# Kernel tuning notes

Measured on AMD Instinct MI355X. Metric: run time of the kernel, lower is better.

## Reference

```python
import jax, jax.numpy as jnp
import numpy as np

EPS = 1e-5  # torch LayerNorm default


def setup_inputs() -> dict:
    key = jax.random.key(0)
    ks = jax.random.split(key, 12)
    N, D, F = 4096, 1024, 4096
    s = 1.0 / np.sqrt(D)
    sf = 1.0 / np.sqrt(F)
    return {
        "embeddings": jax.random.normal(ks[0], (N, D), dtype=jnp.float32),
        "Wq": jax.random.normal(ks[1], (D, D), dtype=jnp.float32) * s,
        "bq": jnp.zeros((D,), jnp.float32),
        "Wk": jax.random.normal(ks[2], (D, D), dtype=jnp.float32) * s,
        "bk": jnp.zeros((D,), jnp.float32),
        "Wv": jax.random.normal(ks[3], (D, D), dtype=jnp.float32) * s,
        "bv": jnp.zeros((D,), jnp.float32),
        "gamma": jnp.ones((D,), jnp.float32),
        "beta": jnp.zeros((D,), jnp.float32),
        "W1": jax.random.normal(ks[4], (D, F), dtype=jnp.float32) * s,
        "b1": jnp.zeros((F,), jnp.float32),
        "W2": jax.random.normal(ks[5], (F, D), dtype=jnp.float32) * sf,
        "b2": jnp.zeros((D,), jnp.float32),
    }


def reference(embeddings, Wq, bq, Wk, bk, Wv, bv, gamma, beta, W1, b1, W2, b2):
    N, D = embeddings.shape
    scale = jnp.sqrt(jnp.float32(D))  # embed_dim ** 0.5
    Q = embeddings @ Wq + bq          # [N, D]
    K = embeddings @ Wk + bk
    V = embeddings @ Wv + bv
    attn = (Q @ K.T) / scale          # [N, N]
    # causal mask: strictly upper triangle -> -inf
    causal = jnp.tril(jnp.ones((N, N), dtype=bool))
    attn = jnp.where(causal, attn, -jnp.inf)
    A = jax.nn.softmax(attn, axis=-1)
    attn_emb = A @ V                  # [N, D]  (dropout = identity at eval)
    # add & norm (LayerNorm over last dim)
    x = attn_emb + embeddings
    mu = jnp.mean(x, axis=-1, keepdims=True)
    var = jnp.mean((x - mu) ** 2, axis=-1, keepdims=True)
    x = (x - mu) / jnp.sqrt(var + EPS) * gamma + beta
    # FFN (no residual after ff in the original module)
    h = jax.nn.relu(x @ W1 + b1)
    return h @ W2 + b2
```

## Files before the change

kernel.cpp:

```cpp
#include <hip/hip_runtime.h>
#include <stdint.h>


using short8 = __attribute__((ext_vector_type(8))) short;
using f32x4  = __attribute__((ext_vector_type(4))) float;

__device__ __forceinline__ uint16_t f2bf(float f) {
  uint32_t u = __builtin_bit_cast(uint32_t, f);
  u += 0x7FFFu + ((u >> 16) & 1u);
  return (uint16_t)(u >> 16);
}

__device__ __forceinline__ void gload_lds16(const uint16_t* g, uint16_t* l) {
  __builtin_amdgcn_global_load_lds(
      (__attribute__((address_space(1))) void*)(void*)g,
      (__attribute__((address_space(3))) void*)l, 16, 0, 0);
}


__global__ __launch_bounds__(256) void gemm_qkv(
    const uint16_t* __restrict__ A, const uint16_t* __restrict__ Bt,
    const float* __restrict__ bias, uint16_t* __restrict__ Cout,
    uint16_t* __restrict__ Vt)
{
  constexpr int BK = 64;
  __shared__ uint16_t As[128 * BK];
  __shared__ uint16_t Bs[128 * BK];
  int id = blockIdx.x;
  int bm = id & 31, bn = id >> 5;
  bool vblk = (bn >= 16);

  int tid  = threadIdx.x;
  int lane = tid & 63;
  int wave = tid >> 6;
  int wm = (wave >> 1) * 64, wn = (wave & 1) * 64;
  int lr = lane & 15, quad = lane >> 4;

  const uint16_t *Ag[4], *Bg[4];
  uint16_t *Al[4], *Bl[4];
#pragma unroll
  for (int s = 0; s < 4; ++s) {
    int c = tid + 256 * s;
    int r = c >> 3, q = (c & 7) ^ (r & 7);
    Ag[s] = A  + (size_t)(bm * 128 + r) * 1024 + q * 8;
    Bg[s] = Bt + (size_t)(bn * 128 + r) * 1024 + q * 8;
    Al[s] = As + c * 8;
    Bl[s] = Bs + c * 8;
  }
  const uint16_t* Fa = vblk ? Bs : As;
  const uint16_t* Fb = vblk ? As : Bs;

  f32x4 acc[4][4] = {};

  for (int k0 = 0; k0 < 1024; k0 += BK) {
    __syncthreads();
#pragma unroll
    for (int s = 0; s < 4; ++s) gload_lds16(Ag[s] + k0, Al[s]);
#pragma unroll
    for (int s = 0; s < 4; ++s) gload_lds16(Bg[s] + k0, Bl[s]);
    __syncthreads();
#pragma unroll
    for (int h = 0; h < 2; ++h) {
      short8 af[4], bfr[4];
      int cc = quad + 4 * h;
#pragma unroll
      for (int i = 0; i < 4; ++i) {
        int r = wm + i * 16 + lr;
        af[i] = *(const short8*)(&Fa[(r * 8 + (cc ^ (r & 7))) * 8]);
      }
#pragma unroll
      for (int j = 0; j < 4; ++j) {
        int r = wn + j * 16 + lr;
        bfr[j] = *(const short8*)(&Fb[(r * 8 + (cc ^ (r & 7))) * 8]);
      }
#pragma unroll
      for (int i = 0; i < 4; ++i)
#pragma unroll
        for (int j = 0; j < 4; ++j)
          acc[i][j] = __builtin_amdgcn_mfma_f32_16x16x32_bf16(af[i], bfr[j], acc[i][j], 0, 0, 0);
    }
  }

  if (vblk) {
#pragma unroll
    for (int i = 0; i < 4; ++i) {
#pragma unroll
      for (int r = 0; r < 4; ++r) {
        int n = bn * 128 + wm + i * 16 + quad * 4 + r;
        float bv = bias[n];
        uint16_t* dst = Vt + (size_t)(n - 2048) * 4096 + bm * 128;
#pragma unroll
        for (int j = 0; j < 4; ++j)
          dst[wn + j * 16 + lr] = f2bf(acc[i][j][r] + bv);
      }
    }
  } else {
    int row0 = bm * 128 + wm + quad * 4;
    int col0 = bn * 128 + wn + lr;
#pragma unroll
    for (int j = 0; j < 4; ++j) {
      int col = col0 + j * 16;
      float bv = bias[col];
#pragma unroll
      for (int i = 0; i < 4; ++i)
#pragma unroll
        for (int r = 0; r < 4; ++r)
          Cout[(size_t)(row0 + i * 16 + r) * 3072 + col] = f2bf(acc[i][j][r] + bv);
    }
  }
}

__global__ __launch_bounds__(256) void gemm_ffn1(
    const uint16_t* __restrict__ A, const uint16_t* __restrict__ Bt,
    const float* __restrict__ bias, uint16_t* __restrict__ Cout)
{
  constexpr int BK = 64;
  __shared__ uint16_t As[128 * BK];
  __shared__ uint16_t Bs[128 * BK];
  int id = blockIdx.x;
  int bm = id & 31, bn = id >> 5;

  int tid  = threadIdx.x;
  int lane = tid & 63;
  int wave = tid >> 6;
  int wm = (wave >> 1) * 64, wn = (wave & 1) * 64;
  int lr = lane & 15, quad = lane >> 4;

  const uint16_t *Ag[4], *Bg[4];
  uint16_t *Al[4], *Bl[4];
#pragma unroll
  for (int s = 0; s < 4; ++s) {
    int c = tid + 256 * s;
    int r = c >> 3, q = (c & 7) ^ (r & 7);
    Ag[s] = A  + (size_t)(bm * 128 + r) * 1024 + q * 8;
    Bg[s] = Bt + (size_t)(bn * 128 + r) * 1024 + q * 8;
    Al[s] = As + c * 8;
    Bl[s] = Bs + c * 8;
  }

  f32x4 acc[4][4] = {};

  for (int k0 = 0; k0 < 1024; k0 += BK) {
    __syncthreads();
#pragma unroll
    for (int s = 0; s < 4; ++s) gload_lds16(Ag[s] + k0, Al[s]);
#pragma unroll
    for (int s = 0; s < 4; ++s) gload_lds16(Bg[s] + k0, Bl[s]);
    __syncthreads();
#pragma unroll
    for (int h = 0; h < 2; ++h) {
      short8 af[4], bfr[4];
      int cc = quad + 4 * h;
#pragma unroll
      for (int i = 0; i < 4; ++i) {
        int r = wm + i * 16 + lr;
        af[i] = *(const short8*)(&As[(r * 8 + (cc ^ (r & 7))) * 8]);
      }
#pragma unroll
      for (int j = 0; j < 4; ++j) {
        int r = wn + j * 16 + lr;
        bfr[j] = *(const short8*)(&Bs[(r * 8 + (cc ^ (r & 7))) * 8]);
      }
#pragma unroll
      for (int i = 0; i < 4; ++i)
#pragma unroll
        for (int j = 0; j < 4; ++j)
          acc[i][j] = __builtin_amdgcn_mfma_f32_16x16x32_bf16(af[i], bfr[j], acc[i][j], 0, 0, 0);
    }
  }

  int row0 = bm * 128 + wm + quad * 4;
  int col0 = bn * 128 + wn + lr;
#pragma unroll
  for (int j = 0; j < 4; ++j) {
    int col = col0 + j * 16;
    float bv = bias[col];
#pragma unroll
    for (int i = 0; i < 4; ++i)
#pragma unroll
      for (int r = 0; r < 4; ++r)
        Cout[(size_t)(row0 + i * 16 + r) * 4096 + col] =
            f2bf(fmaxf(acc[i][j][r] + bv, 0.0f));
  }
}

__global__ __launch_bounds__(256) void gemm_s(
    const uint16_t* __restrict__ Qm, const uint16_t* __restrict__ Km,
    uint16_t* __restrict__ Sb, float* __restrict__ lvec,
    int lda, int ldb, int ldc, float scale)
{
  constexpr int BK = 64;
  __shared__ uint16_t As[64 * BK];
  __shared__ uint16_t Bs[128 * BK];
  int id = blockIdx.x;
  int i64 = id & 63, bn = id >> 6;
  if (bn > (i64 >> 1)) return;

  int tid  = threadIdx.x;
  int lane = tid & 63;
  int wave = tid >> 6;
  int wm = (wave >> 1) * 32, wn = (wave & 1) * 64;
  int lr = lane & 15, quad = lane >> 4;

  const uint16_t *Ag[2], *Bg[4];
  uint16_t *Al[2], *Bl[4];
#pragma unroll
  for (int s = 0; s < 2; ++s) {
    int c = tid + 256 * s;
    int r = c >> 3, q = (c & 7) ^ (r & 7);
    Ag[s] = Qm + (size_t)(i64 * 64 + r) * lda + q * 8;
    Al[s] = As + c * 8;
  }
#pragma unroll
  for (int s = 0; s < 4; ++s) {
    int c = tid + 256 * s;
    int r = c >> 3, q = (c & 7) ^ (r & 7);
    Bg[s] = Km + (size_t)(bn * 128 + r) * ldb + q * 8;
    Bl[s] = Bs + c * 8;
  }

  f32x4 acc[2][4] = {};

  for (int k0 = 0; k0 < 1024; k0 += BK) {
    __syncthreads();
#pragma unroll
    for (int s = 0; s < 2; ++s) gload_lds16(Ag[s] + k0, Al[s]);
#pragma unroll
    for (int s = 0; s < 4; ++s) gload_lds16(Bg[s] + k0, Bl[s]);
    __syncthreads();
#pragma unroll
    for (int h = 0; h < 2; ++h) {
      short8 af[2], bfr[4];
      int cc = quad + 4 * h;
#pragma unroll
      for (int i = 0; i < 2; ++i) {
        int r = wm + i * 16 + lr;
        af[i] = *(const short8*)(&As[(r * 8 + (cc ^ (r & 7))) * 8]);
      }
#pragma unroll
      for (int j = 0; j < 4; ++j) {
        int r = wn + j * 16 + lr;
        bfr[j] = *(const short8*)(&Bs[(r * 8 + (cc ^ (r & 7))) * 8]);
      }
#pragma unroll
      for (int i = 0; i < 2; ++i)
#pragma unroll
        for (int j = 0; j < 4; ++j)
          acc[i][j] = __builtin_amdgcn_mfma_f32_16x16x32_bf16(af[i], bfr[j], acc[i][j], 0, 0, 0);
    }
  }

  int row0 = i64 * 64 + wm + quad * 4;
  int col0 = bn * 128 + wn + lr;
#pragma unroll
  for (int i = 0; i < 2; ++i) {
#pragma unroll
    for (int r = 0; r < 4; ++r) {
      int row = row0 + i * 16 + r;
      float s = 0.0f;
#pragma unroll
      for (int j = 0; j < 4; ++j) {
        int col = col0 + j * 16;
        float v = (col <= row) ? __expf(acc[i][j][r] * scale) : 0.0f;
        Sb[(size_t)row * ldc + col] = f2bf(v);
        s += v;
      }
#pragma unroll
      for (int o = 8; o > 0; o >>= 1) s += __shfl_xor(s, o, 64);
      if (lr == 0) unsafeAtomicAdd(&lvec[row], s);
    }
  }
}

__global__ __launch_bounds__(256) void gemm_o(
    const uint16_t* __restrict__ Sb, const uint16_t* __restrict__ Vt,
    float* __restrict__ Opart)
{
  constexpr int BK = 64;
  __shared__ uint16_t As[128 * BK];
  __shared__ uint16_t Bs[128 * BK];
  int id = blockIdx.x;
  int bn = id / 80, p = id % 80;
  int c, bm;
  if      (p < 25) { c = 0; bm = 7 + p; }
  else if (p < 49) { c = 1; bm = 8 + (p - 25); }
  else if (p < 65) { c = 2; bm = 16 + (p - 49); }
  else if (p < 73) { c = 3; bm = 24 + (p - 65); }
  else             { c = 0; bm = 79 - p; }
  int klo = c << 10;
  int khi = (bm + 1) << 7; if (khi > ((c + 1) << 10)) khi = (c + 1) << 10;

  int tid  = threadIdx.x;
  int lane = tid & 63;
  int wave = tid >> 6;
  int wm = (wave >> 1) * 64, wn = (wave & 1) * 64;
  int lr = lane & 15, quad = lane >> 4;

  const uint16_t *Ag[4], *Bg[4];
  uint16_t *Al[4], *Bl[4];
#pragma unroll
  for (int s = 0; s < 4; ++s) {
    int cch = tid + 256 * s;
    int r = cch >> 3, q = (cch & 7) ^ (r & 7);
    Ag[s] = Sb + (size_t)(bm * 128 + r) * 4096 + q * 8;
    Bg[s] = Vt + (size_t)(bn * 128 + r) * 4096 + q * 8;
    Al[s] = As + cch * 8;
    Bl[s] = Bs + cch * 8;
  }

  f32x4 acc[4][4] = {};

  for (int k0 = klo; k0 < khi; k0 += BK) {
    __syncthreads();
#pragma unroll
    for (int s = 0; s < 4; ++s) gload_lds16(Ag[s] + k0, Al[s]);
#pragma unroll
    for (int s = 0; s < 4; ++s) gload_lds16(Bg[s] + k0, Bl[s]);
    __syncthreads();
#pragma unroll
    for (int h = 0; h < 2; ++h) {
      short8 af[4], bfr[4];
      int cc = quad + 4 * h;
#pragma unroll
      for (int i = 0; i < 4; ++i) {
        int r = wm + i * 16 + lr;
        af[i] = *(const short8*)(&As[(r * 8 + (cc ^ (r & 7))) * 8]);
      }
#pragma unroll
      for (int j = 0; j < 4; ++j) {
        int r = wn + j * 16 + lr;
        bfr[j] = *(const short8*)(&Bs[(r * 8 + (cc ^ (r & 7))) * 8]);
      }
#pragma unroll
      for (int i = 0; i < 4; ++i)
#pragma unroll
        for (int j = 0; j < 4; ++j)
          acc[i][j] = __builtin_amdgcn_mfma_f32_16x16x32_bf16(af[i], bfr[j], acc[i][j], 0, 0, 0);
    }
  }

  float* P = Opart + (size_t)c * 4194304;
  int row0 = bm * 128 + wm + quad * 4;
  int col0 = bn * 128 + wn + lr;
#pragma unroll
  for (int j = 0; j < 4; ++j)
#pragma unroll
    for (int i = 0; i < 4; ++i)
#pragma unroll
      for (int r = 0; r < 4; ++r)
        P[(size_t)(row0 + i * 16 + r) * 1024 + col0 + j * 16] = acc[i][j][r];
}

__global__ __launch_bounds__(256) void gemm_ffn2(
    const uint16_t* __restrict__ A, const uint16_t* __restrict__ Bt,
    float* __restrict__ Cout)
{
  constexpr int BK = 64;
  __shared__ uint16_t As[128 * BK];
  __shared__ uint16_t Bs[64 * BK];
  int id = blockIdx.x;
  int bn = id >> 6, p = id & 63;
  int bm = p >> 1, half = p & 1;
  int klo = half ? 2048 : 0, khi = half ? 4096 : 2048;

  int tid  = threadIdx.x;
  int lane = tid & 63;
  int wave = tid >> 6;
  int wm = (wave & 1) * 64, wn = (wave >> 1) * 32;
  int lr = lane & 15, quad = lane >> 4;

  const uint16_t *Ag[4], *Bg[2];
  uint16_t *Al[4], *Bl[2];
#pragma unroll
  for (int s = 0; s < 4; ++s) {
    int c = tid + 256 * s;
    int r = c >> 3, q = (c & 7) ^ (r & 7);
    Ag[s] = A + (size_t)(bm * 128 + r) * 4096 + q * 8;
    Al[s] = As + c * 8;
  }
#pragma unroll
  for (int s = 0; s < 2; ++s) {
    int c = tid + 256 * s;
    int r = c >> 3, q = (c & 7) ^ (r & 7);
    Bg[s] = Bt + (size_t)(bn * 64 + r) * 4096 + q * 8;
    Bl[s] = Bs + c * 8;
  }

  f32x4 acc[4][2] = {};

  for (int k0 = klo; k0 < khi; k0 += BK) {
    __syncthreads();
#pragma unroll
    for (int s = 0; s < 4; ++s) gload_lds16(Ag[s] + k0, Al[s]);
#pragma unroll
    for (int s = 0; s < 2; ++s) gload_lds16(Bg[s] + k0, Bl[s]);
    __syncthreads();
#pragma unroll
    for (int h = 0; h < 2; ++h) {
      short8 af[4], bfr[2];
      int cc = quad + 4 * h;
#pragma unroll
      for (int i = 0; i < 4; ++i) {
        int r = wm + i * 16 + lr;
        af[i] = *(const short8*)(&As[(r * 8 + (cc ^ (r & 7))) * 8]);
      }
#pragma unroll
      for (int j = 0; j < 2; ++j) {
        int r = wn + j * 16 + lr;
        bfr[j] = *(const short8*)(&Bs[(r * 8 + (cc ^ (r & 7))) * 8]);
      }
#pragma unroll
      for (int i = 0; i < 4; ++i)
#pragma unroll
        for (int j = 0; j < 2; ++j)
          acc[i][j] = __builtin_amdgcn_mfma_f32_16x16x32_bf16(af[i], bfr[j], acc[i][j], 0, 0, 0);
    }
  }

  int row0 = bm * 128 + wm + quad * 4;
  int col0 = bn * 64 + wn + lr;
#pragma unroll
  for (int j = 0; j < 2; ++j)
#pragma unroll
    for (int i = 0; i < 4; ++i)
#pragma unroll
      for (int r = 0; r < 4; ++r) {
        size_t idx = (size_t)(row0 + i * 16 + r) * 1024 + col0 + j * 16;
        unsafeAtomicAdd(&Cout[idx], acc[i][j][r]);
      }
}

__device__ __forceinline__ float block_sum(float v, float* red) {
#pragma unroll
  for (int o = 32; o > 0; o >>= 1) v += __shfl_xor(v, o, 64);
  if ((threadIdx.x & 63) == 0) red[threadIdx.x >> 6] = v;
  __syncthreads();
  v = red[0] + red[1] + red[2] + red[3];
  __syncthreads();
  return v;
}

__global__ __launch_bounds__(256) void add_layernorm(
    const float* __restrict__ P, const float* __restrict__ l,
    const float* __restrict__ emb, const float* __restrict__ gamma,
    const float* __restrict__ beta, uint16_t* __restrict__ xB)
{
  __shared__ float red[4];
  int i = blockIdx.x, tid = threadIdx.x;
  float inv_l = 1.0f / l[i];
  int nc = (i >> 10) + 1;
  float s0 = 0.0f, s1 = 0.0f, s2 = 0.0f, s3 = 0.0f;
  for (int c = 0; c < nc; ++c) {
    float4 a = ((const float4*)(P + (size_t)c * 4194304 + (size_t)i * 1024))[tid];
    s0 += a.x; s1 += a.y; s2 += a.z; s3 += a.w;
  }
  float4 b = ((const float4*)(emb + (size_t)i * 1024))[tid];
  float x0 = s0 * inv_l + b.x, x1 = s1 * inv_l + b.y;
  float x2 = s2 * inv_l + b.z, x3 = s3 * inv_l + b.w;
  float mu = block_sum(x0 + x1 + x2 + x3, red) * (1.0f / 1024.0f);
  float d0 = x0 - mu, d1 = x1 - mu, d2 = x2 - mu, d3 = x3 - mu;
  float var = block_sum(d0 * d0 + d1 * d1 + d2 * d2 + d3 * d3, red) * (1.0f / 1024.0f);
  float rs = rsqrtf(var + 1e-5f);
  float4 g  = ((const float4*)gamma)[tid];
  float4 be = ((const float4*)beta)[tid];
  ushort4 o;
  o.x = f2bf(d0 * rs * g.x + be.x);
  o.y = f2bf(d1 * rs * g.y + be.y);
  o.z = f2bf(d2 * rs * g.z + be.z);
  o.w = f2bf(d3 * rs * g.w + be.w);
  ((ushort4*)(xB + (size_t)i * 1024))[tid] = o;
}

__global__ __launch_bounds__(256) void prep(
    const float* __restrict__ emb, const float* __restrict__ Wq,
    const float* __restrict__ Wk, const float* __restrict__ Wv,
    const float* __restrict__ W1, const float* __restrict__ W2,
    const float* __restrict__ bq, const float* __restrict__ bk,
    const float* __restrict__ bv, const float* __restrict__ b2,
    uint16_t* __restrict__ embB, uint16_t* __restrict__ WqkvT,
    uint16_t* __restrict__ W1T, uint16_t* __restrict__ W2T,
    float* __restrict__ bqkv, float* __restrict__ lvec,
    float* __restrict__ outInit)
{
  __shared__ float tile[32][33];
  int b = blockIdx.x, tid = threadIdx.x;
  if (b < 4096) {
    int idx = b * 256 + tid;
    float4 v = ((const float4*)emb)[idx];
    ushort4 o; o.x = f2bf(v.x); o.y = f2bf(v.y); o.z = f2bf(v.z); o.w = f2bf(v.w);
    ((ushort4*)embB)[idx] = o;
    return;
  }
  int tx = tid & 31, ty = tid >> 5;
  if (b < 7168) {
    int local = b - 4096;
    const float* in = (local < 1024) ? Wq : (local < 2048) ? Wk : Wv;
    uint16_t* o = WqkvT + (size_t)(local >> 10) * 1048576;
    int rem = local & 1023;
    int r0 = (rem >> 5) * 32, c0 = (rem & 31) * 32;
#pragma unroll
    for (int r = 0; r < 32; r += 8)
      tile[ty + r][tx] = in[(size_t)(r0 + ty + r) * 1024 + c0 + tx];
    __syncthreads();
#pragma unroll
    for (int r = 0; r < 32; r += 8)
      o[(size_t)(c0 + ty + r) * 1024 + r0 + tx] = f2bf(tile[tx][ty + r]);
    return;
  }
  if (b < 11264) {
    int local = b - 7168;
    int c0 = (local & 127) * 32, r0 = (local >> 7) * 32;
#pragma unroll
    for (int r = 0; r < 32; r += 8)
      tile[ty + r][tx] = W1[(size_t)(r0 + ty + r) * 4096 + c0 + tx];
    __syncthreads();
#pragma unroll
    for (int r = 0; r < 32; r += 8)
      W1T[(size_t)(c0 + ty + r) * 1024 + r0 + tx] = f2bf(tile[tx][ty + r]);
    return;
  }
  if (b < 15360) {
    int local = b - 11264;
    int c0 = (local & 31) * 32, r0 = (local >> 5) * 32;
#pragma unroll
    for (int r = 0; r < 32; r += 8)
      tile[ty + r][tx] = W2[(size_t)(r0 + ty + r) * 1024 + c0 + tx];
    __syncthreads();
#pragma unroll
    for (int r = 0; r < 32; r += 8)
      W2T[(size_t)(c0 + ty + r) * 4096 + r0 + tx] = f2bf(tile[tx][ty + r]);
    return;
  }
  if (b < 15372) {
    int i = (b - 15360) * 256 + tid;
    bqkv[i] = (i < 1024) ? bq[i] : (i < 2048) ? bk[i - 1024] : bv[i - 2048];
    return;
  }
  if (b == 15372) {
#pragma unroll
    for (int i = tid; i < 4096; i += 256) lvec[i] = 0.0f;
    return;
  }
  {
    int row = b - 15373;
    float4 bv4 = ((const float4*)b2)[tid];
    ((float4*)(outInit + (size_t)row * 1024))[tid] = bv4;
  }
}

extern "C" void kernel_launch(void* const* d_in, const int* in_sizes, int n_in,
                              void* d_out, int out_size, void* d_ws, size_t ws_size,
                              hipStream_t stream) {
  const float* emb   = (const float*)d_in[0];
  const float* Wq    = (const float*)d_in[1];
  const float* bq    = (const float*)d_in[2];
  const float* Wk    = (const float*)d_in[3];
  const float* bk    = (const float*)d_in[4];
  const float* Wv    = (const float*)d_in[5];
  const float* bv    = (const float*)d_in[6];
  const float* gamma = (const float*)d_in[7];
  const float* beta  = (const float*)d_in[8];
  const float* W1    = (const float*)d_in[9];
  const float* b1    = (const float*)d_in[10];
  const float* W2    = (const float*)d_in[11];
  const float* b2    = (const float*)d_in[12];

  char* w = (char*)d_ws;
  const size_t MB = 1ull << 20;
  uint16_t* embB  = (uint16_t*)(w + 0 * MB);
  uint16_t* WqkvT = (uint16_t*)(w + 8 * MB);
  uint16_t* W1T   = (uint16_t*)(w + 14 * MB);
  uint16_t* W2T   = (uint16_t*)(w + 22 * MB);
  float*    bqkv  = (float*)(w + 30 * MB);
  float*    lvec  = (float*)(w + 30 * MB + 65536);
  uint16_t* QKVb  = (uint16_t*)(w + 31 * MB);
  uint16_t* Vt    = (uint16_t*)(w + 55 * MB);
  uint16_t* Sb    = (uint16_t*)(w + 63 * MB);
  uint16_t* hB    = (uint16_t*)(w + 63 * MB);
  float*    Opart = (float*)(w + 95 * MB);
  uint16_t* xB    = (uint16_t*)(w + 0 * MB);

  prep<<<19469, 256, 0, stream>>>(emb, Wq, Wk, Wv, W1, W2, bq, bk, bv, b2,
                                  embB, WqkvT, W1T, W2T, bqkv, lvec,
                                  (float*)d_out);

  gemm_qkv<<<768, 256, 0, stream>>>(embB, WqkvT, bqkv, QKVb, Vt);
  const uint16_t* Qb = QKVb;
  const uint16_t* Kb = QKVb + 1024;

  gemm_s<<<2048, 256, 0, stream>>>(Qb, Kb, Sb, lvec, 3072, 3072, 4096, 0.03125f);

  gemm_o<<<640, 256, 0, stream>>>(Sb, Vt, Opart);

  add_layernorm<<<4096, 256, 0, stream>>>(Opart, lvec, emb, gamma, beta, xB);

  gemm_ffn1<<<1024, 256, 0, stream>>>(xB, W1T, b1, hB);

  gemm_ffn2<<<1024, 256, 0, stream>>>(hB, W2T, (float*)d_out);
}
```

Measured before the change: 336.5 us.

## Replace split-K atomic FFN2 with full-K tiles and fused bias store

The second FFN GEMM no longer splits K in half with atomic adds into an output pre-filled with b2. Each block now computes a 64x128 output tile over the full K range and writes the result plus bias directly, which also lets the prep kernel drop its output-initialization blocks. This removes the atomic traffic and the extra output-init pass. The cost is half as many blocks (512), which lowers parallelism on a GPU with many CUs, and each block runs a K loop twice as long.

```diff
diff --git a/kernel.cpp b/kernel.cpp
--- a/kernel.cpp
+++ b/kernel.cpp
@@ -353,81 +353,80 @@
 
 __global__ __launch_bounds__(256) void gemm_ffn2(
     const uint16_t* __restrict__ A, const uint16_t* __restrict__ Bt,
-    float* __restrict__ Cout)
+    const float* __restrict__ bias, float* __restrict__ Cout)
 {
   constexpr int BK = 64;
-  __shared__ uint16_t As[128 * BK];
-  __shared__ uint16_t Bs[64 * BK];
+  __shared__ uint16_t As[64 * BK];
+  __shared__ uint16_t Bs[128 * BK];
   int id = blockIdx.x;
-  int bn = id >> 6, p = id & 63;
-  int bm = p >> 1, half = p & 1;
-  int klo = half ? 2048 : 0, khi = half ? 4096 : 2048;
+  int bn = id >> 6, bm = id & 63;
 
   int tid  = threadIdx.x;
   int lane = tid & 63;
   int wave = tid >> 6;
-  int wm = (wave & 1) * 64, wn = (wave >> 1) * 32;
+  int wm = (wave >> 1) * 32, wn = (wave & 1) * 64;
   int lr = lane & 15, quad = lane >> 4;
 
-  const uint16_t *Ag[4], *Bg[2];
-  uint16_t *Al[4], *Bl[2];
+  const uint16_t *Ag[2], *Bg[4];
+  uint16_t *Al[2], *Bl[4];
+#pragma unroll
+  for (int s = 0; s < 2; ++s) {
+    int c = tid + 256 * s;
+    int r = c >> 3, q = (c & 7) ^ (r & 7);
+    Ag[s] = A + (size_t)(bm * 64 + r) * 4096 + q * 8;
+    Al[s] = As + c * 8;
+  }
 #pragma unroll
   for (int s = 0; s < 4; ++s) {
     int c = tid + 256 * s;
     int r = c >> 3, q = (c & 7) ^ (r & 7);
-    Ag[s] = A + (size_t)(bm * 128 + r) * 4096 + q * 8;
-    Al[s] = As + c * 8;
-  }
-#pragma unroll
-  for (int s = 0; s < 2; ++s) {
-    int c = tid + 256 * s;
-    int r = c >> 3, q = (c & 7) ^ (r & 7);
-    Bg[s] = Bt + (size_t)(bn * 64 + r) * 4096 + q * 8;
+    Bg[s] = Bt + (size_t)(bn * 128 + r) * 4096 + q * 8;
     Bl[s] = Bs + c * 8;
   }
 
-  f32x4 acc[4][2] = {};
-
-  for (int k0 = klo; k0 < khi; k0 += BK) {
-    __syncthreads();
-#pragma unroll
-    for (int s = 0; s < 4; ++s) gload_lds16(Ag[s] + k0, Al[s]);
-#pragma unroll
-    for (int s = 0; s < 2; ++s) gload_lds16(Bg[s] + k0, Bl[s]);
+  f32x4 acc[2][4] = {};
+
+  for (int k0 = 0; k0 < 4096; k0 += BK) {
+    __syncthreads();
+#pragma unroll
+    for (int s = 0; s < 2; ++s) gload_lds16(Ag[s] + k0, Al[s]);
+#pragma unroll
+    for (int s = 0; s < 4; ++s) gload_lds16(Bg[s] + k0, Bl[s]);
     __syncthreads();
 #pragma unroll
     for (int h = 0; h < 2; ++h) {
-      short8 af[4], bfr[2];
+      short8 af[2], bfr[4];
       int cc = quad + 4 * h;
 #pragma unroll
-      for (int i = 0; i < 4; ++i) {
+      for (int i = 0; i < 2; ++i) {
         int r = wm + i * 16 + lr;
         af[i] = *(const short8*)(&As[(r * 8 + (cc ^ (r & 7))) * 8]);
       }
 #pragma unroll
-      for (int j = 0; j < 2; ++j) {
+      for (int j = 0; j < 4; ++j) {
         int r = wn + j * 16 + lr;
         bfr[j] = *(const short8*)(&Bs[(r * 8 + (cc ^ (r & 7))) * 8]);
       }
 #pragma unroll
-      for (int i = 0; i < 4; ++i)
-#pragma unroll
-        for (int j = 0; j < 2; ++j)
+      for (int i = 0; i < 2; ++i)
+#pragma unroll
+        for (int j = 0; j < 4; ++j)
           acc[i][j] = __builtin_amdgcn_mfma_f32_16x16x32_bf16(af[i], bfr[j], acc[i][j], 0, 0, 0);
     }
   }
 
-  int row0 = bm * 128 + wm + quad * 4;
-  int col0 = bn * 64 + wn + lr;
-#pragma unroll
-  for (int j = 0; j < 2; ++j)
-#pragma unroll
-    for (int i = 0; i < 4; ++i)
-#pragma unroll
-      for (int r = 0; r < 4; ++r) {
-        size_t idx = (size_t)(row0 + i * 16 + r) * 1024 + col0 + j * 16;
-        unsafeAtomicAdd(&Cout[idx], acc[i][j][r]);
-      }
+  int row0 = bm * 64 + wm + quad * 4;
+  int col0 = bn * 128 + wn + lr;
+#pragma unroll
+  for (int j = 0; j < 4; ++j) {
+    int col = col0 + j * 16;
+    float bv = bias[col];
+#pragma unroll
+    for (int i = 0; i < 2; ++i)
+#pragma unroll
+      for (int r = 0; r < 4; ++r)
+        Cout[(size_t)(row0 + i * 16 + r) * 1024 + col] = acc[i][j][r] + bv;
+  }
 }
 
 __device__ __forceinline__ float block_sum(float v, float* red) {
@@ -476,11 +475,10 @@
     const float* __restrict__ Wk, const float* __restrict__ Wv,
     const float* __restrict__ W1, const float* __restrict__ W2,
     const float* __restrict__ bq, const float* __restrict__ bk,
-    const float* __restrict__ bv, const float* __restrict__ b2,
-    uint16_t* __restrict__ embB, uint16_t* __restrict__ WqkvT,
-    uint16_t* __restrict__ W1T, uint16_t* __restrict__ W2T,
-    float* __restrict__ bqkv, float* __restrict__ lvec,
-    float* __restrict__ outInit)
+    const float* __restrict__ bv, uint16_t* __restrict__ embB,
+    uint16_t* __restrict__ WqkvT, uint16_t* __restrict__ W1T,
+    uint16_t* __restrict__ W2T, float* __restrict__ bqkv,
+    float* __restrict__ lvec)
 {
   __shared__ float tile[32][33];
   int b = blockIdx.x, tid = threadIdx.x;
@@ -536,15 +534,9 @@
     bqkv[i] = (i < 1024) ? bq[i] : (i < 2048) ? bk[i - 1024] : bv[i - 2048];
     return;
   }
-  if (b == 15372) {
+  {
 #pragma unroll
     for (int i = tid; i < 4096; i += 256) lvec[i] = 0.0f;
-    return;
-  }
-  {
-    int row = b - 15373;
-    float4 bv4 = ((const float4*)b2)[tid];
-    ((float4*)(outInit + (size_t)row * 1024))[tid] = bv4;
   }
 }
 
@@ -580,9 +572,8 @@
   float*    Opart = (float*)(w + 95 * MB);
   uint16_t* xB    = (uint16_t*)(w + 0 * MB);
 
-  prep<<<19469, 256, 0, stream>>>(emb, Wq, Wk, Wv, W1, W2, bq, bk, bv, b2,
-                                  embB, WqkvT, W1T, W2T, bqkv, lvec,
-                                  (float*)d_out);
+  prep<<<15373, 256, 0, stream>>>(emb, Wq, Wk, Wv, W1, W2, bq, bk, bv,
+                                  embB, WqkvT, W1T, W2T, bqkv, lvec);
 
   gemm_qkv<<<768, 256, 0, stream>>>(embB, WqkvT, bqkv, QKVb, Vt);
   const uint16_t* Qb = QKVb;
@@ -596,5 +587,5 @@
 
   gemm_ffn1<<<1024, 256, 0, stream>>>(xB, W1T, b1, hB);
 
-  gemm_ffn2<<<1024, 256, 0, stream>>>(hB, W2T, (float*)d_out);
-}
+  gemm_ffn2<<<512, 256, 0, stream>>>(hB, W2T, b2, (float*)d_out);
+}
```

Result: no change. 337.7 us (+0.3%).
